# Performance work log

Measured on AMD Instinct MI355X. Metric: run time of the kernel, lower is better.

Reference implementation:

```python
import jax, jax.numpy as jnp
import numpy as np

B, S, F = 2048, 512, 64   # batch, seq_len, input_features
H = 32                    # LSTM_HIDDEN_SIZE
H1, H2 = 32, 16           # HIDDEN_SIZES
O = 3                     # output_features


def setup_inputs() -> dict:
    key = jax.random.key(0)
    ks = jax.random.split(key, 10)
    sc = lambda n: 1.0 / np.sqrt(n)
    x = jax.random.normal(ks[0], (B, S, F), dtype=jnp.float32)
    # LSTM kernels, gate order (i, f, g, o); input kernel has no bias (flax LSTMCell),
    # hidden kernel carries the bias.
    Wx = jax.random.normal(ks[1], (F, 4 * H), dtype=jnp.float32) * sc(F)
    Wh = jax.random.normal(ks[2], (H, 4 * H), dtype=jnp.float32) * sc(H)
    b = jnp.zeros((4 * H,), dtype=jnp.float32)
    # MLP head: 32 -> 32 -> 16 -> 3 with leaky_relu between hidden layers
    W1 = jax.random.normal(ks[3], (H, H1), dtype=jnp.float32) * sc(H)
    b1 = jnp.zeros((H1,), dtype=jnp.float32)
    W2 = jax.random.normal(ks[4], (H1, H2), dtype=jnp.float32) * sc(H1)
    b2 = jnp.zeros((H2,), dtype=jnp.float32)
    Wo = jax.random.normal(ks[5], (H2, O), dtype=jnp.float32) * sc(H2)
    bo = jnp.zeros((O,), dtype=jnp.float32)
    return {"x": x, "Wx": Wx, "Wh": Wh, "b": b,
            "W1": W1, "b1": b1, "W2": W2, "b2": b2, "Wo": Wo, "bo": bo}


def _lstm_last_hidden(x, Wx, Wh, b):
    # Precompute input-to-gate projections for all timesteps (same math,
    # hoists the [B,S,F]x[F,4H] GEMM out of the scan).
    bsz = x.shape[0]
    h_dim = Wh.shape[0]
    xg = jnp.einsum('bsf,fg->sbg', x, Wx)  # [S, B, 4H], time-major for scan

    def step(carry, xg_t):
        c, h = carry
        z = xg_t + h @ Wh + b               # [B, 4H]
        i, f, g, o = jnp.split(z, 4, axis=-1)
        i = jax.nn.sigmoid(i)
        f = jax.nn.sigmoid(f)
        g = jnp.tanh(g)
        o = jax.nn.sigmoid(o)
        c_new = f * c + i * g
        h_new = o * jnp.tanh(c_new)
        return (c_new, h_new), None

    c0 = jnp.zeros((bsz, h_dim), dtype=x.dtype)
    h0 = jnp.zeros((bsz, h_dim), dtype=x.dtype)
    (c_T, h_T), _ = jax.lax.scan(step, (c0, h0), xg)
    return h_T  # last hidden state, matches x[1][:, -1, :]


def reference(x, Wx, Wh, b, W1, b1, W2, b2, Wo, bo):
    h = _lstm_last_hidden(x, Wx, Wh, b)        # [B, H]
    a = jax.nn.leaky_relu(h @ W1 + b1)         # [B, 32]
    a = jax.nn.leaky_relu(a @ W2 + b2)         # [B, 16]
    return a @ Wo + bo                         # [B, O]
```

## Files before the change

kernel.cpp:

```cpp
#include <hip/hip_runtime.h>

#define S_  512
#define F_  64
#define H_  32
#define GQ  128
#define BT  8
#define NB  256

#define XS  72
#define HS  40
#define GS  33

typedef __attribute__((ext_vector_type(8))) short bf16x8;
typedef __attribute__((ext_vector_type(4))) float f32x4;

__device__ __forceinline__ unsigned pack_split(float f) {
    unsigned u  = __builtin_bit_cast(unsigned, f);
    unsigned hi = (u + 0x7FFFu + ((u >> 16) & 1u)) & 0xFFFF0000u;
    float    fl = f - __builtin_bit_cast(float, hi);
    unsigned ul = __builtin_bit_cast(unsigned, fl);
    unsigned lo = (ul + 0x7FFFu + ((ul >> 16) & 1u)) >> 16;
    return hi | lo;
}

__device__ __forceinline__ unsigned short bf16_rne(float f) {
    unsigned u = __builtin_bit_cast(unsigned, f);
    return (unsigned short)((u + 0x7FFFu + ((u >> 16) & 1u)) >> 16);
}

__device__ __forceinline__ float sigm(float z) {
    return __builtin_amdgcn_rcpf(1.0f + __expf(-z));
}
__device__ __forceinline__ float tanh_f(float z) {
    return 2.0f * __builtin_amdgcn_rcpf(1.0f + __expf(-2.0f * z)) - 1.0f;
}

#define MFMA(A, B, C) __builtin_amdgcn_mfma_f32_16x16x32_bf16(A, B, C, 0, 0, 0)

__global__ __launch_bounds__(512, 1)
void lstm_mfma_kernel(const float* __restrict__ x,  const float* __restrict__ Wx,
                      const float* __restrict__ Wh, const float* __restrict__ bg,
                      const float* __restrict__ W1, const float* __restrict__ b1,
                      const float* __restrict__ W2, const float* __restrict__ b2,
                      const float* __restrict__ Wo, const float* __restrict__ bo,
                      float* __restrict__ out)
{
    const int tid = threadIdx.x;
    const int w   = tid >> 6;
    const int L   = tid & 63;
    const int c16 = L & 15;
    const int kg  = L >> 4;
    const int bb  = blockIdx.x * BT;
    const int jj  = (w << 2) + kg;

    const int gcol = ((c16 & 3) << 5) + (w << 2) + (c16 >> 2);

    __shared__ __align__(16) unsigned short xh[4][16][XS];
    __shared__ __align__(16) unsigned short hh[2][16][HS];
    __shared__ float Hd[3][BT][GS];

    bf16x8 whh_, whl_, wx0h, wx0l, wx1h, wx1l;
#pragma unroll
    for (int i = 0; i < 8; ++i) {
        unsigned p = pack_split(Wx[(kg * 8 + i) * GQ + gcol]);
        wx0h[i] = (short)(unsigned short)(p >> 16);
        wx0l[i] = (short)(unsigned short)(p & 0xFFFFu);
        p = pack_split(Wx[(32 + kg * 8 + i) * GQ + gcol]);
        wx1h[i] = (short)(unsigned short)(p >> 16);
        wx1l[i] = (short)(unsigned short)(p & 0xFFFFu);
        p = pack_split(Wh[(kg * 8 + i) * GQ + gcol]);
        whh_[i] = (short)(unsigned short)(p >> 16);
        whl_[i] = (short)(unsigned short)(p & 0xFFFFu);
    }
    f32x4 biasC;
#pragma unroll
    for (int r = 0; r < 4; ++r) biasC[r] = bg[r * 32 + jj];
    const f32x4 zeroC = {0.f, 0.f, 0.f, 0.f};

    for (int i = tid; i < 2 * 16 * (HS / 2); i += 512)
        ((unsigned*)&hh[0][0][0])[i] = 0u;

    const int srow = tid >> 5;
    const int sfp  = tid & 31;
    const int sdt  = srow >> 3;
    const float* xsrc = x + (size_t)(bb + (srow & 7)) * S_ * F_ + 2 * sfp;
    {
#pragma unroll
        for (int tt = 0; tt < 2; ++tt) {
            float2 v = *(const float2*)(xsrc + (size_t)(2 * tt + sdt) * F_);
            *(unsigned*)&xh[tt][srow][2 * sfp] =
                (unsigned)bf16_rne(v.x) | ((unsigned)bf16_rne(v.y) << 16);
        }
    }
    float2 xvA = *(const float2*)(xsrc + (size_t)(4 + sdt) * F_);
    float2 xvB = *(const float2*)(xsrc + (size_t)(6 + sdt) * F_);
    __syncthreads();

    f32x4 xzA, xz1s;
    {
        bf16x8 bxh0 = *(const bf16x8*)&xh[0][c16][kg * 8];
        bf16x8 bxh1 = *(const bf16x8*)&xh[0][c16][32 + kg * 8];
        f32x4 b0 = MFMA(wx0h, bxh0, biasC);
        f32x4 b2 = MFMA(wx0l, bxh0, zeroC);
        b0 = MFMA(wx1h, bxh1, b0);
        b2 = MFMA(wx1l, bxh1, b2);
        f32x4 xs = b0 + b2;
        xzA = xs;
#pragma unroll
        for (int r = 0; r < 4; ++r) xz1s[r] = __shfl_xor(xs[r], 8);
    }

    float cc = 0.0f;

#define DSTEP(TD, XV) {                                                        \
    const int td = (TD);                                                       \
    int tl = td + 4; if (tl > 255) tl = 255;                                   \
    float2 xnext = *(const float2*)(xsrc + (size_t)(2 * tl + sdt) * F_);       \
                              \
    bf16x8 bhh = *(const bf16x8*)&hh[1][c16][kg * 8];                          \
    f32x4 a0 = MFMA(whh_, bhh, xzA);                                           \
    f32x4 a2 = MFMA(whl_, bhh, zeroC);                                         \
    f32x4 z = a0 + a2;                                                         \
    float iv = sigm(z[0]), fv = sigm(z[1]);                                    \
    float gv = tanh_f(z[2]), ov = sigm(z[3]);                                  \
    cc = fmaf(fv, cc, iv * gv);                                                \
    float hv = ov * tanh_f(cc);                                                \
    if (c16 < 8) hh[0][c16][jj] = bf16_rne(hv);                                \
           \
    f32x4 xzA_n, xz1s_n;                                                       \
    {                                                                          \
        const int s1 = (td + 1) & 3;                                           \
        bf16x8 bxh0 = *(const bf16x8*)&xh[s1][c16][kg * 8];                    \
        bf16x8 bxh1 = *(const bf16x8*)&xh[s1][c16][32 + kg * 8];               \
        f32x4 b0 = MFMA(wx0h, bxh0, biasC);                                    \
        f32x4 b2 = MFMA(wx0l, bxh0, zeroC);                                    \
        b0 = MFMA(wx1h, bxh1, b0);                                             \
        b2 = MFMA(wx1l, bxh1, b2);                                             \
        f32x4 xs = b0 + b2;                                                    \
        xzA_n = xs;                                                            \
        _Pragma("unroll")                                                      \
        for (int r = 0; r < 4; ++r) xz1s_n[r] = __shfl_xor(xs[r], 8);          \
    }                                                                          \
    __syncthreads();                                    \
                              \
    bhh = *(const bf16x8*)&hh[0][c16][kg * 8];                                 \
    a0 = MFMA(whh_, bhh, xz1s);                                                \
    a2 = MFMA(whl_, bhh, zeroC);                                               \
    z = a0 + a2;                                                               \
    iv = sigm(z[0]); fv = sigm(z[1]);                                          \
    gv = tanh_f(z[2]); ov = sigm(z[3]);                                        \
    cc = fmaf(fv, cc, iv * gv);                                                \
    hv = ov * tanh_f(cc);                                                      \
    if (c16 < 8) {                                                             \
        hh[1][c16][jj] = bf16_rne(hv);                                         \
        if (td == 255) Hd[0][c16][jj] = hv;                                    \
    }                                                                          \
                              \
    *(unsigned*)&xh[(td + 2) & 3][srow][2 * sfp] =                             \
        (unsigned)bf16_rne(XV.x) | ((unsigned)bf16_rne(XV.y) << 16);           \
    XV = xnext;                                                                \
    xzA = xzA_n; xz1s = xz1s_n;                                                \
    __syncthreads();                      \
}

    for (int qd = 0; qd < 128; ++qd) {
        DSTEP(2 * qd,     xvA)
        DSTEP(2 * qd + 1, xvB)
    }
#undef DSTEP

    __syncthreads();

    if (tid < 256) {
        int rb = tid >> 5, n = tid & 31;
        float a = b1[n];
#pragma unroll
        for (int k = 0; k < 32; ++k) a = fmaf(Hd[0][rb][k], W1[k * 32 + n], a);
        a = (a > 0.0f) ? a : 0.01f * a;
        Hd[1][rb][n] = a;
    }
    __syncthreads();
    if (tid < 128) {
        int rb = tid >> 4, n = tid & 15;
        float a = b2[n];
#pragma unroll
        for (int k = 0; k < 32; ++k) a = fmaf(Hd[1][rb][k], W2[k * 16 + n], a);
        a = (a > 0.0f) ? a : 0.01f * a;
        Hd[2][rb][n] = a;
    }
    __syncthreads();
    if (tid < 24) {
        int rb = tid / 3, n = tid - rb * 3;
        float a = bo[n];
#pragma unroll
        for (int k = 0; k < 16; ++k) a = fmaf(Hd[2][rb][k], Wo[k * 3 + n], a);
        out[(size_t)(bb + rb) * 3 + n] = a;
    }
}

extern "C" void kernel_launch(void* const* d_in, const int* in_sizes, int n_in,
                              void* d_out, int out_size, void* d_ws, size_t ws_size,
                              hipStream_t stream) {
    const float* x  = (const float*)d_in[0];
    const float* Wx = (const float*)d_in[1];
    const float* Wh = (const float*)d_in[2];
    const float* bg = (const float*)d_in[3];
    const float* W1 = (const float*)d_in[4];
    const float* b1 = (const float*)d_in[5];
    const float* W2 = (const float*)d_in[6];
    const float* b2 = (const float*)d_in[7];
    const float* Wo = (const float*)d_in[8];
    const float* bo = (const float*)d_in[9];
    float* out = (float*)d_out;

    hipLaunchKernelGGL(lstm_mfma_kernel, dim3(NB), dim3(512), 0, stream,
                       x, Wx, Wh, bg, W1, b1, W2, b2, Wo, bo, out);
}
```

Baseline: 169.6 us.

## Halve batch tile per block to double grid size and allow two blocks per CU

Reduces the batch rows per block from 8 to 4, doubling the number of blocks to 512, and raises launch bounds to allow two resident blocks per CU. The x staging is reworked to one float per thread, padding rows in the shared x buffer are zeroed, and the h-writeback and MLP head bounds are adjusted to the smaller tile. The goal is to fill all CUs and overlap two serial recurrence chains per CU. The cost is that half of each MFMA's batch columns are wasted and register pressure is capped by the two-block occupancy target.

After: 254.0 us. 49.8% more time.

```diff
diff --git a/kernel.cpp b/kernel.cpp
--- a/kernel.cpp
+++ b/kernel.cpp
@@ -4,8 +4,8 @@
 #define F_  64
 #define H_  32
 #define GQ  128
-#define BT  8
-#define NB  256
+#define BT  4
+#define NB  512
 
 #define XS  72
 #define HS  40
@@ -37,7 +37,7 @@
 
 #define MFMA(A, B, C) __builtin_amdgcn_mfma_f32_16x16x32_bf16(A, B, C, 0, 0, 0)
 
-__global__ __launch_bounds__(512, 1)
+__global__ __launch_bounds__(512, 2)
 void lstm_mfma_kernel(const float* __restrict__ x,  const float* __restrict__ Wx,
                       const float* __restrict__ Wh, const float* __restrict__ bg,
                       const float* __restrict__ W1, const float* __restrict__ b1,
@@ -79,21 +79,25 @@
 
     for (int i = tid; i < 2 * 16 * (HS / 2); i += 512)
         ((unsigned*)&hh[0][0][0])[i] = 0u;
-
-    const int srow = tid >> 5;
-    const int sfp  = tid & 31;
-    const int sdt  = srow >> 3;
-    const float* xsrc = x + (size_t)(bb + (srow & 7)) * S_ * F_ + 2 * sfp;
-    {
-#pragma unroll
-        for (int tt = 0; tt < 2; ++tt) {
-            float2 v = *(const float2*)(xsrc + (size_t)(2 * tt + sdt) * F_);
-            *(unsigned*)&xh[tt][srow][2 * sfp] =
-                (unsigned)bf16_rne(v.x) | ((unsigned)bf16_rne(v.y) << 16);
-        }
-    }
-    float2 xvA = *(const float2*)(xsrc + (size_t)(4 + sdt) * F_);
-    float2 xvB = *(const float2*)(xsrc + (size_t)(6 + sdt) * F_);
+    for (int i = tid; i < 4 * 8 * (XS / 2); i += 512) {
+        int slot = i / (8 * (XS / 2));
+        int rem  = i - slot * 8 * (XS / 2);
+        int rr   = rem / (XS / 2);
+        int row  = 4 + (rr & 3) + ((rr >> 2) << 3);
+        int col  = rem % (XS / 2);
+        ((unsigned*)&xh[slot][row][0])[col] = 0u;
+    }
+
+    const int sbat = (tid >> 6) & 3;
+    const int sdt  = tid >> 8;
+    const int srow = sbat + (sdt << 3);
+    const int sfc  = tid & 63;
+    const float* xsrc = x + (size_t)(bb + sbat) * S_ * F_ + sfc;
+#pragma unroll
+    for (int tt = 0; tt < 2; ++tt)
+        xh[tt][srow][sfc] = bf16_rne(xsrc[(size_t)(2 * tt + sdt) * F_]);
+    float xvA = xsrc[(size_t)(4 + sdt) * F_];
+    float xvB = xsrc[(size_t)(6 + sdt) * F_];
     __syncthreads();
 
     f32x4 xzA, xz1s;
@@ -115,7 +119,7 @@
 #define DSTEP(TD, XV) {                                                        \
     const int td = (TD);                                                       \
     int tl = td + 4; if (tl > 255) tl = 255;                                   \
-    float2 xnext = *(const float2*)(xsrc + (size_t)(2 * tl + sdt) * F_);       \
+    float xnext = xsrc[(size_t)(2 * tl + sdt) * F_];                           \
                               \
     bf16x8 bhh = *(const bf16x8*)&hh[1][c16][kg * 8];                          \
     f32x4 a0 = MFMA(whh_, bhh, xzA);                                           \
@@ -125,7 +129,7 @@
     float gv = tanh_f(z[2]), ov = sigm(z[3]);                                  \
     cc = fmaf(fv, cc, iv * gv);                                                \
     float hv = ov * tanh_f(cc);                                                \
-    if (c16 < 8) hh[0][c16][jj] = bf16_rne(hv);                                \
+    if (c16 < 4) hh[0][c16][jj] = bf16_rne(hv);                                \
            \
     f32x4 xzA_n, xz1s_n;                                                       \
     {                                                                          \
@@ -151,13 +155,12 @@
     gv = tanh_f(z[2]); ov = sigm(z[3]);                                        \
     cc = fmaf(fv, cc, iv * gv);                                                \
     hv = ov * tanh_f(cc);                                                      \
-    if (c16 < 8) {                                                             \
+    if (c16 < 4) {                                                             \
         hh[1][c16][jj] = bf16_rne(hv);                                         \
         if (td == 255) Hd[0][c16][jj] = hv;                                    \
     }                                                                          \
                               \
-    *(unsigned*)&xh[(td + 2) & 3][srow][2 * sfp] =                             \
-        (unsigned)bf16_rne(XV.x) | ((unsigned)bf16_rne(XV.y) << 16);           \
+    xh[(td + 2) & 3][srow][sfc] = bf16_rne(XV);                                \
     XV = xnext;                                                                \
     xzA = xzA_n; xz1s = xz1s_n;                                                \
     __syncthreads();                      \
@@ -171,7 +174,7 @@
 
     __syncthreads();
 
-    if (tid < 256) {
+    if (tid < BT * 32) {
         int rb = tid >> 5, n = tid & 31;
         float a = b1[n];
 #pragma unroll
@@ -180,7 +183,7 @@
         Hd[1][rb][n] = a;
     }
     __syncthreads();
-    if (tid < 128) {
+    if (tid < BT * 16) {
         int rb = tid >> 4, n = tid & 15;
         float a = b2[n];
 #pragma unroll
@@ -189,7 +192,7 @@
         Hd[2][rb][n] = a;
     }
     __syncthreads();
-    if (tid < 24) {
+    if (tid < BT * 3) {
         int rb = tid / 3, n = tid - rb * 3;
         float a = bo[n];
 #pragma unroll
```
